# Optimization experiments

Hardware: AMD Instinct MI355X
Metric: run time of the kernel (lower is better)

## Reference

```python
import jax, jax.numpy as jnp
import numpy as np

BODY_EDGES = [(0, 2), (0, 5), (2, 7), (5, 8), (11, 12), (0, 11), (0, 12), (7, 11), (8, 12), (11, 13), (13, 15), (12, 14), (14, 16), (11, 23), (12, 24), (23, 24), (11, 24), (12, 23)]
N_JOINTS = 33
N_FEAT = 52
HIDDEN = 128
BN_EPS = 1e-5


def _make_adj():
    a = np.eye(N_JOINTS, dtype=np.float32)
    for i, j in BODY_EDGES:
        a[i, j] = 1.0
        a[j, i] = 1.0
    deg = np.clip(a.sum(1), 1.0, None)
    d = deg ** -0.5
    return jnp.asarray(d[:, None] * a * d[None, :])


def setup_inputs() -> dict:
    key = jax.random.key(0)
    ks = iter(jax.random.split(key, 40))
    B, T = 64, 256
    def lin(k, i, o):
        return jax.random.normal(k, (i, o), jnp.float32) / np.sqrt(i)
    inp = {
        'x': jax.random.normal(next(ks), (B, T, N_JOINTS, N_FEAT), jnp.float32),
        'adj': _make_adj(),
        # layer 0: in 52 -> out 128 (has skip linear)
        'W0': lin(next(ks), N_FEAT, HIDDEN), 'b0': jax.random.normal(next(ks), (HIDDEN,)) * 0.02,
        'S0': lin(next(ks), N_FEAT, HIDDEN), 'sb0': jax.random.normal(next(ks), (HIDDEN,)) * 0.02,
        'g0': 1.0 + 0.1 * jax.random.normal(next(ks), (HIDDEN,)), 'be0': 0.1 * jax.random.normal(next(ks), (HIDDEN,)),
        'm0': 0.1 * jax.random.normal(next(ks), (HIDDEN,)), 'v0': 1.0 + 0.1 * jax.random.uniform(next(ks), (HIDDEN,)),
        # layers 1,2: 128 -> 128 (identity skip)
        'W1': lin(next(ks), HIDDEN, HIDDEN), 'b1': jax.random.normal(next(ks), (HIDDEN,)) * 0.02,
        'g1': 1.0 + 0.1 * jax.random.normal(next(ks), (HIDDEN,)), 'be1': 0.1 * jax.random.normal(next(ks), (HIDDEN,)),
        'm1': 0.1 * jax.random.normal(next(ks), (HIDDEN,)), 'v1': 1.0 + 0.1 * jax.random.uniform(next(ks), (HIDDEN,)),
        'W2': lin(next(ks), HIDDEN, HIDDEN), 'b2': jax.random.normal(next(ks), (HIDDEN,)) * 0.02,
        'g2': 1.0 + 0.1 * jax.random.normal(next(ks), (HIDDEN,)), 'be2': 0.1 * jax.random.normal(next(ks), (HIDDEN,)),
        'm2': 0.1 * jax.random.normal(next(ks), (HIDDEN,)), 'v2': 1.0 + 0.1 * jax.random.uniform(next(ks), (HIDDEN,)),
        # temporal attention MLP: 128 -> 128 -> 1
        'tW1': lin(next(ks), HIDDEN, HIDDEN), 'tb1': jax.random.normal(next(ks), (HIDDEN,)) * 0.02,
        'tW2': lin(next(ks), HIDDEN, 1), 'tb2': jax.random.normal(next(ks), (1,)) * 0.02,
    }
    return inp


def _gcn(h, adj, W, b, g, be, m, v, skip):
    # adjacency mix: [B*T, J, D_in]
    a = jnp.einsum('nm,bmd->bnd', adj, h)
    z = a @ W + b
    z = (z - m) * jax.lax.rsqrt(v + BN_EPS) * g + be  # eval-mode BatchNorm1d
    return jax.nn.gelu(z, approximate=False) + skip


def reference(x, adj, W0, b0, S0, sb0, g0, be0, m0, v0,
              W1, b1, g1, be1, m1, v1,
              W2, b2, g2, be2, m2, v2,
              tW1, tb1, tW2, tb2):
    B, T, J, Fd = x.shape
    h = x.reshape(B * T, J, Fd)
    h = _gcn(h, adj, W0, b0, g0, be0, m0, v0, h @ S0 + sb0)
    h = _gcn(h, adj, W1, b1, g1, be1, m1, v1, h)
    h = _gcn(h, adj, W2, b2, g2, be2, m2, v2, h)
    # dropout inactive (eval mode)
    xt = h.mean(axis=1).reshape(B, T, -1)                  # [B, T, H]
    score = jax.nn.gelu(xt @ tW1 + tb1, approximate=False) @ tW2 + tb2  # [B, T, 1]
    attn = jax.nn.softmax(score, axis=1)
    return (xt * attn).sum(axis=1)                         # [B, H]
```

## Files before the change

kernel.cpp:

```cpp
#include <hip/hip_runtime.h>
#include <hip/hip_bf16.h>
#include <math.h>


#define NJ 33
#define NF 52
#define NH 128
#define NT 256
#define NB 64
#define NSAMP (NB*NT)
#define SPB 2
#define NBLKS (NSAMP/SPB)
#define HSTR 136
#define PSTR 40

typedef unsigned short u16;
typedef _Float16 f16;
typedef f16   half8 __attribute__((ext_vector_type(8)));
typedef f16   h2    __attribute__((ext_vector_type(2)));
typedef float f32x4 __attribute__((ext_vector_type(4)));

#define HO_W0    0
#define HO_S0    8192
#define HO_W1    16384
#define HO_W2    32768
#define HO_TW1   49152
#define HO_ADJ32 65536
#define H_TOTAL  66560
#define FO_BASE  (H_TOTAL/2)
#define FO_A0    (FO_BASE+0)
#define FO_SB0   (FO_BASE+768)
#define FO_TB1   (FO_BASE+896)
#define FO_TW2   (FO_BASE+1024)
#define FO_FLG   (FO_BASE+1152)
#define FO_XT    (FO_BASE+1280)
#define FO_SC    (FO_XT + NSAMP*NH)

__device__ __forceinline__ float bf2f(u16 u) { return __uint_as_float(((unsigned)u) << 16); }
__device__ __forceinline__ float ldv(const void* p, long i, int f) {
    float r;
    if (f) r = bf2f(((const u16*)p)[i]);
    else   r = ((const float*)p)[i];
    return r;
}
__device__ int detect_bf16(const void* p) {
    const u16* q = (const u16*)p;
    int nz = 0, ok = 0;
#pragma unroll
    for (int k = 0; k < 64; k++) {
        u16 u = q[k];
        if (u & 0x7FFF) {
            nz++;
            int e = (u >> 7) & 0xFF;
            ok += (e >= 0x40 && e <= 0xBF) ? 1 : 0;
        }
    }
    return (nz == 0) || (ok * 20 >= nz * 19);
}

__device__ __forceinline__ float gelu_c(float x) {
    float xc = fminf(fmaxf(x, -8.f), 8.f);
    float u  = xc * fmaf(xc * xc, 0.10294324f, 2.3022082f);
#if __has_builtin(__builtin_amdgcn_exp2f)
    float e  = __builtin_amdgcn_exp2f(u);
#else
    float e  = exp2f(u);
#endif
#if __has_builtin(__builtin_amdgcn_rcpf)
    float tt = (e - 1.f) * __builtin_amdgcn_rcpf(e + 1.f);
#else
    float tt = (e - 1.f) / (e + 1.f);
#endif
    float hx = 0.5f * x;
    return fmaf(hx, tt, hx);
}

#define MFMA16(a, b, c) __builtin_amdgcn_mfma_f32_16x16x32_f16(a, b, c, 0, 0, 0)

__global__ __launch_bounds__(256) void prep(
    const void* x, const void* adj,
    const void* W0, const void* b0, const void* S0, const void* sb0,
    const void* g0, const void* be0, const void* m0, const void* v0,
    const void* W1, const void* b1, const void* g1, const void* be1, const void* m1, const void* v1,
    const void* W2, const void* b2, const void* g2, const void* be2, const void* m2, const void* v2,
    const void* tW1, const void* tb1, const void* tW2,
    void* ws)
{
    f16* H = (f16*)ws; float* F = (float*)ws;
    const int bi = blockIdx.x, t = threadIdx.x;

    if (bi < 64) {
        const void* src; int dst, kt, nt, Kvalid, Kd;
        if (bi < 16)      { src = W1;  dst = HO_W1;  kt = (bi>>2)&3;    nt = bi&3;      Kvalid = 128; Kd = 128; }
        else if (bi < 32) { src = W2;  dst = HO_W2;  kt = ((bi-16)>>2); nt = (bi-16)&3; Kvalid = 128; Kd = 128; }
        else if (bi < 48) { src = tW1; dst = HO_TW1; kt = ((bi-32)>>2); nt = (bi-32)&3; Kvalid = 128; Kd = 128; }
        else if (bi < 56) { src = W0;  dst = HO_W0;  kt = ((bi-48)>>2); nt = (bi-48)&3; Kvalid = NF;  Kd = 64;  }
        else              { src = S0;  dst = HO_S0;  kt = ((bi-56)>>2); nt = (bi-56)&3; Kvalid = NF;  Kd = 64;  }
        const int flag = detect_bf16(src);
        __shared__ float tile[32][33];
        const int tx = t & 31, ty = t >> 5;
#pragma unroll
        for (int r = 0; r < 4; r++) {
            int k = kt*32 + ty + r*8;
            int n = nt*32 + tx;
            tile[ty + r*8][tx] = (k < Kvalid) ? ldv(src, (long)k*128 + n, flag) : 0.f;
        }
        __syncthreads();
#pragma unroll
        for (int r = 0; r < 4; r++) {
            int n = nt*32 + ty + r*8;
            int k = kt*32 + tx;
            H[dst + n*Kd + k] = (f16)tile[tx][ty + r*8];
        }
    } else {
        if (t == 0) ((int*)F)[FO_FLG] = detect_bf16(x);
        if (t < 128) {
            int c = t;
            {
                float g = ldv(g0,c,detect_bf16(g0)), be = ldv(be0,c,detect_bf16(be0));
                float m = ldv(m0,c,detect_bf16(m0)), v = ldv(v0,c,detect_bf16(v0));
                float b = ldv(b0,c,detect_bf16(b0));
                float A = g * rsqrtf(v + 1e-5f);
                F[FO_A0 + 0*256 + c] = A; F[FO_A0 + 0*256 + 128 + c] = (b - m)*A + be;
            }
            {
                float g = ldv(g1,c,detect_bf16(g1)), be = ldv(be1,c,detect_bf16(be1));
                float m = ldv(m1,c,detect_bf16(m1)), v = ldv(v1,c,detect_bf16(v1));
                float b = ldv(b1,c,detect_bf16(b1));
                float A = g * rsqrtf(v + 1e-5f);
                F[FO_A0 + 1*256 + c] = A; F[FO_A0 + 1*256 + 128 + c] = (b - m)*A + be;
            }
            {
                float g = ldv(g2,c,detect_bf16(g2)), be = ldv(be2,c,detect_bf16(be2));
                float m = ldv(m2,c,detect_bf16(m2)), v = ldv(v2,c,detect_bf16(v2));
                float b = ldv(b2,c,detect_bf16(b2));
                float A = g * rsqrtf(v + 1e-5f);
                F[FO_A0 + 2*256 + c] = A; F[FO_A0 + 2*256 + 128 + c] = (b - m)*A + be;
            }
            F[FO_SB0 + c] = ldv(sb0, c, detect_bf16(sb0));
            F[FO_TB1 + c] = ldv(tb1, c, detect_bf16(tb1));
            F[FO_TW2 + c] = ldv(tW2, c, detect_bf16(tW2));
        }
        const int fA = detect_bf16(adj);
        for (int i = t; i < 1024; i += 256) {
            int r = i >> 5, c = i & 31;
            float v = (r < 25 && c < 25) ? ldv(adj, (long)r*NJ + c, fA) : 0.f;
            H[HO_ADJ32 + i] = (f16)v;
        }
    }
}

#define ADJEPI_W(L, WRHB) {                                                     \
    f32x4 zac[2][2];                                                            \
    _Pragma("unroll")                                                           \
    for (int fF = 0; fF < 2; fF++) {                                            \
        half8 bz = *(const half8*)(Pt + (fF*128 + c)*PSTR + q*8);               \
        zac[fF][0] = MFMA16(afadj0, bz, z4);                                    \
        zac[fF][1] = MFMA16(afadj1, bz, z4);                                    \
    }                                                                           \
    const float Av = rA[L], Dv = rD[L];                                         \
    _Pragma("unroll")                                                           \
    for (int fF = 0; fF < 2; fF++) {                                            \
        _Pragma("unroll")                                                       \
        for (int m2 = 0; m2 < 2; m2++) {                                        \
            _Pragma("unroll")                                                   \
            for (int r4 = 0; r4 < 4; r4++) {                                    \
                float zv = (m2 == 0) ? zac[fF][0][r4]                           \
                         : (jlt[r4] ? zac[fF][1][r4] : acc[2*fF+1][r4]);        \
                float hnew = gelu_c(fmaf(zv, Av, Dv)) + hz[fF][m2][r4];         \
                hz[fF][m2][r4] = hnew;                                          \
                if (WRHB)                                                       \
                    hb[((2*fF+m2)*16 + q*4 + r4)*HSTR + c] = (f16)hnew;         \
            }                                                                   \
        }                                                                       \
        {                                                                       \
            float hnew = gelu_c(fmaf(acc[4][fF], Av, Dv)) + h32[fF];            \
            h32[fF] = (q == 0) ? hnew : 0.f;                                    \
            if (WRHB && q == 0)                                                 \
                hb[(64 + fF)*HSTR + c] = (f16)hnew;                             \
        }                                                                       \
    }                                                                           \
}

#define PTWRITE_W(ACC)                                                          \
    _Pragma("unroll")                                                           \
    for (int mt = 0; mt < 4; mt++) {                                            \
        const int fF = mt >> 1;                                                 \
        const int jb = (mt & 1) * 16;                                           \
        f16* pp = Pt + (fF*128 + c)*PSTR;                                       \
        _Pragma("unroll")                                                       \
        for (int r2 = 0; r2 < 4; r2 += 2) {                                     \
            int j0 = jb + q*4 + r2;                                             \
            if (j0 + 1 < 25) {                                                  \
                h2 v2w = { (f16)ACC[mt][r2], (f16)ACC[mt][r2+1] };              \
                *(h2*)(pp + j0) = v2w;                                          \
            } else if (j0 < 25) {                                               \
                pp[j0] = (f16)ACC[mt][r2];                                      \
            }                                                                   \
        }                                                                       \
    }

#define GEMM128_W(WOFF)                                                         \
    {                                                                           \
        half8 bf[4];                                                            \
        _Pragma("unroll")                                                       \
        for (int ks = 0; ks < 4; ks++)                                          \
            bf[ks] = *(const half8*)(HW + (WOFF) + c*128 + ks*32 + q*8);        \
        _Pragma("unroll")                                                       \
        for (int mt = 0; mt < 5; mt++) acc[mt] = z4;                            \
        _Pragma("unroll")                                                       \
        for (int mt = 0; mt < 5; mt++) {                                        \
            const int m = mt*16 + ml;                                           \
            _Pragma("unroll")                                                   \
            for (int ks = 0; ks < 4; ks++) {                                    \
                half8 af = *(const half8*)(hb + m*HSTR + ks*32 + q*8);          \
                acc[mt] = MFMA16(af, bf[ks], acc[mt]);                          \
            }                                                                   \
        }                                                                       \
    }

#define GCN_W_BODY                                                              \
    float* xtb = (float*)Pt;                                                    \
    const f16* HW = (const f16*)ws;                                             \
    float* F = (float*)ws;                                                      \
    float* xt_g = F + FO_XT;                                                    \
    float* sc_g = F + FO_SC;                                                    \
    const int t = threadIdx.x, lane = t & 63, wv = t >> 6;                      \
    const int q = lane >> 4, ml = lane & 15;                                    \
    const int c = wv * 16 + ml;                                                 \
    const f32x4 z4 = {0.f, 0.f, 0.f, 0.f};                                      \
    const bool jlt[4] = { q <= 2, q <= 1, q <= 1, q <= 1 };                     \
    const half8 zero8 = {(f16)0.f,(f16)0.f,(f16)0.f,(f16)0.f,(f16)0.f,(f16)0.f,(f16)0.f,(f16)0.f}; \
    {                                                                           \
        int fF = t >> 8, rem = t & 255, n = rem >> 1, chh = rem & 1;            \
        *(half8*)(Pt + (fF*128 + n)*PSTR + 24 + chh*8) = zero8;                 \
    }                                                                           \
    float rA[3], rD[3];                                                         \
    _Pragma("unroll")                                                           \
    for (int L = 0; L < 3; L++) {                                               \
        rA[L] = F[FO_A0 + L*256 + c];                                           \
        rD[L] = F[FO_A0 + L*256 + 128 + c];                                     \
    }                                                                           \
    const float sb0v = F[FO_SB0 + c];                                           \
    half8 afadj0 = *(const half8*)(HW + HO_ADJ32 + ml*32 + q*8);                \
    half8 afadj1 = *(const half8*)(HW + HO_ADJ32 + (16+ml)*32 + q*8);           \
    __syncthreads();                                                            \
    {                                                                           \
        const int fX = ((const int*)F)[FO_FLG];                                 \
        const long xb = (long)blockIdx.x * (SPB * NJ * NF);                     \
        _Pragma("unroll 1")                                                     \
        for (int it = 0; it < 2; it++) {                                        \
            int g = t + it * 512;                                               \
            if (g < 66 * 8) {                                                   \
                int r = g >> 3, blk = g & 7;                                    \
                int fF = (r >= 33) ? 1 : 0;                                     \
                int j = r - 33 * fF;                                            \
                int fr = (j < 32) ? (fF * 32 + j) : (64 + fF);                  \
                half8 o;                                                        \
                if (!fX) {                                                      \
                    const float* base = (const float*)x + xb + (long)r * NF + blk * 8; \
                    if (blk < 6) {                                              \
                        float4 v0 = *(const float4*)base;                       \
                        float4 v1 = *(const float4*)(base + 4);                 \
                        o[0]=(f16)v0.x; o[1]=(f16)v0.y; o[2]=(f16)v0.z; o[3]=(f16)v0.w; \
                        o[4]=(f16)v1.x; o[5]=(f16)v1.y; o[6]=(f16)v1.z; o[7]=(f16)v1.w; \
                    } else if (blk == 6) {                                      \
                        float4 v0 = *(const float4*)base;                       \
                        o = zero8;                                              \
                        o[0]=(f16)v0.x; o[1]=(f16)v0.y; o[2]=(f16)v0.z; o[3]=(f16)v0.w; \
                    } else o = zero8;                                           \
                } else {                                                        \
                    long rb = xb + (long)r * NF;                                \
                    _Pragma("unroll")                                           \
                    for (int i = 0; i < 8; i++) {                               \
                        int cx = blk * 8 + i;                                   \
                        o[i] = (f16)(cx < NF ? bf2f(((const u16*)x)[rb + cx]) : 0.f); \
                    }                                                           \
                }                                                               \
                *(half8*)(hb + fr * HSTR + blk * 8) = o;                        \
            }                                                                   \
        }                                                                       \
    }                                                                           \
    __syncthreads();                                                            \
    f32x4 acc[5];                                                               \
    float hz[2][2][4];                                                          \
    float h32[2];                                                               \
    {                                                                           \
        half8 bw[2], bs[2];                                                     \
        _Pragma("unroll")                                                       \
        for (int ks = 0; ks < 2; ks++) {                                        \
            bw[ks] = *(const half8*)(HW + HO_W0 + c*64 + ks*32 + q*8);          \
            bs[ks] = *(const half8*)(HW + HO_S0 + c*64 + ks*32 + q*8);          \
        }                                                                       \
        f32x4 acs[5];                                                           \
        _Pragma("unroll")                                                       \
        for (int mt = 0; mt < 5; mt++) { acc[mt] = z4; acs[mt] = z4; }          \
        _Pragma("unroll")                                                       \
        for (int mt = 0; mt < 5; mt++) {                                        \
            const int m = mt*16 + ml;                                           \
            half8 a0 = *(const half8*)(hb + m*HSTR + q*8);                      \
            half8 a1 = *(const half8*)(hb + m*HSTR + 32 + q*8);                 \
            acc[mt] = MFMA16(a0, bw[0], acc[mt]);                               \
            acc[mt] = MFMA16(a1, bw[1], acc[mt]);                               \
            acs[mt] = MFMA16(a0, bs[0], acs[mt]);                               \
            acs[mt] = MFMA16(a1, bs[1], acs[mt]);                               \
        }                                                                       \
        __syncthreads();                                                        \
        PTWRITE_W(acc)                                                          \
        _Pragma("unroll")                                                       \
        for (int fF = 0; fF < 2; fF++)                                          \
            _Pragma("unroll")                                                   \
            for (int m2 = 0; m2 < 2; m2++)                                      \
                _Pragma("unroll")                                               \
                for (int r4 = 0; r4 < 4; r4++)                                  \
                    hz[fF][m2][r4] = acs[2*fF+m2][r4] + sb0v;                   \
        _Pragma("unroll")                                                       \
        for (int fF = 0; fF < 2; fF++)                                          \
            h32[fF] = (q == 0) ? (acs[4][fF] + sb0v) : 0.f;                     \
    }                                                                           \
    ADJEPI_W(0, 1)                                                              \
    __syncthreads();                                                            \
    GEMM128_W(HO_W1)                                                            \
    __syncthreads();                                                            \
    PTWRITE_W(acc)                                                              \
    ADJEPI_W(1, 1)                                                              \
    __syncthreads();                                                            \
    GEMM128_W(HO_W2)                                                            \
    __syncthreads();                                                            \
    PTWRITE_W(acc)                                                              \
    ADJEPI_W(2, 0)                                                              \
    __syncthreads();                                                            \
    _Pragma("unroll")                                                           \
    for (int fF = 0; fF < 2; fF++) {                                            \
        float s = h32[fF];                                                      \
        _Pragma("unroll")                                                       \
        for (int m2 = 0; m2 < 2; m2++)                                          \
            _Pragma("unroll")                                                   \
            for (int r4 = 0; r4 < 4; r4++) s += hz[fF][m2][r4];                 \
        s += __shfl_xor(s, 16, 64);                                             \
        s += __shfl_xor(s, 32, 64);                                             \
        float xtc = s * (1.0f / 33.0f);                                         \
        if (q == 0) {                                                           \
            xtb[fF * 128 + c] = xtc;                                            \
            xt_g[((long)blockIdx.x * SPB + fF) * NH + c] = xtc;                 \
        }                                                                       \
    }                                                                           \
    __syncthreads();                                                            \
    {                                                                           \
        float r = 0.f;                                                          \
        if (t < 256) {                                                          \
            const int fF = t >> 7, ch = t & 127;                                \
            float u = 0.f;                                                      \
            _Pragma("unroll")                                                   \
            for (int kk = 0; kk < 16; kk++) {                                   \
                half8 wv8 = *(const half8*)(HW + HO_TW1 + ch*128 + kk*8);       \
                _Pragma("unroll")                                               \
                for (int i = 0; i < 8; i++)                                     \
                    u = fmaf(xtb[fF*128 + kk*8 + i], (float)wv8[i], u);         \
            }                                                                   \
            r = gelu_c(u + F[FO_TB1 + ch]) * F[FO_TW2 + ch];                    \
        }                                                                       \
        _Pragma("unroll")                                                       \
        for (int off = 32; off > 0; off >>= 1) r += __shfl_xor(r, off, 64);     \
        if (lane == 0 && wv < 4) rbuf4[wv] = r;                                 \
        __syncthreads();                                                        \
        if (t == 0) {                                                           \
            sc_g[blockIdx.x * SPB + 0] = rbuf4[0] + rbuf4[1];                   \
            sc_g[blockIdx.x * SPB + 1] = rbuf4[2] + rbuf4[3];                   \
        }                                                                       \
    }

__global__ __launch_bounds__(512) void gcn_mfma_w(const void* __restrict__ x,
                                                  void* __restrict__ ws)
{
    __shared__ __align__(16) f16 hb[80 * HSTR];
    __shared__ __align__(16) f16 Pt[2 * 128 * PSTR];
    __shared__ float rbuf4[4];
    GCN_W_BODY
}

__global__ __launch_bounds__(512, 8) void gcn_mfma_w73(const void* __restrict__ x,
                                                       void* __restrict__ ws)
{
    __shared__ __align__(16) f16 hb[73 * HSTR];
    __shared__ __align__(16) f16 Pt[2 * 128 * PSTR];
    __shared__ float rbuf4[4];
    GCN_W_BODY
}

__global__ __launch_bounds__(256) void attn_pool(
    const int* __restrict__ flg,
    const float* __restrict__ xt_ws, const float* __restrict__ score_ws,
    void* __restrict__ out)
{
    __shared__ float ew[NT];
    __shared__ float red[8];
    __shared__ float pb[256];
    const int t = threadIdx.x, lane = t & 63, wv = t >> 6;
    const int b = blockIdx.x >> 2, qr = blockIdx.x & 3;

    float sv = score_ws[b * NT + t];
    float m = sv;
#pragma unroll
    for (int off = 32; off > 0; off >>= 1) m = fmaxf(m, __shfl_xor(m, off, 64));
    if (lane == 0) red[wv] = m;
    __syncthreads();
    float mx = fmaxf(fmaxf(red[0], red[1]), fmaxf(red[2], red[3]));
    float e = __expf(sv - mx);
    ew[t] = e;
    float d = e;
#pragma unroll
    for (int off = 32; off > 0; off >>= 1) d += __shfl_xor(d, off, 64);
    if (lane == 0) red[4 + wv] = d;
    __syncthreads();
    float den = red[4] + red[5] + red[6] + red[7];

    const int cl = t & 31, ch = t >> 5;
    const int c = qr * 32 + cl;
    float a = 0.f;
#pragma unroll 4
    for (int i = ch * 32; i < ch * 32 + 32; i++)
        a = fmaf(ew[i], xt_ws[((long)b * NT + i) * NH + c], a);
    pb[t] = a;
    __syncthreads();
    if (t < 128) pb[t] += pb[t + 128];
    __syncthreads();
    if (t < 64) pb[t] += pb[t + 64];
    __syncthreads();
    if (t < 32) {
        float r = (pb[t] + pb[t + 32]) / den;
        if (*flg) ((__hip_bfloat16*)out)[b * NH + qr * 32 + t] = __float2bfloat16(r);
        else      ((float*)out)[b * NH + qr * 32 + t] = r;
    }
}

extern "C" void kernel_launch(void* const* d_in, const int* in_sizes, int n_in,
                              void* d_out, int out_size, void* d_ws, size_t ws_size,
                              hipStream_t stream) {
    static int use_73 = -1;
    if (use_73 < 0) {
        hipFuncAttributes a{};
        use_73 = 0;
        if (hipFuncGetAttributes(&a, reinterpret_cast<const void*>(gcn_mfma_w73)) == hipSuccess
            && a.numRegs > 0 && a.numRegs <= 64
            && a.localSizeBytes == 0)
            use_73 = 1;
    }
    prep<<<65, 256, 0, stream>>>(
        d_in[0], d_in[1],
        d_in[2], d_in[3], d_in[4], d_in[5],
        d_in[6], d_in[7], d_in[8], d_in[9],
        d_in[10], d_in[11], d_in[12], d_in[13], d_in[14], d_in[15],
        d_in[16], d_in[17], d_in[18], d_in[19], d_in[20], d_in[21],
        d_in[22], d_in[23], d_in[24],
        d_ws);
    if (use_73) gcn_mfma_w73<<<NBLKS, 512, 0, stream>>>(d_in[0], d_ws);
    else        gcn_mfma_w<<<NBLKS, 512, 0, stream>>>(d_in[0], d_ws);
    float* F = (float*)d_ws;
    attn_pool<<<NB * 4, 256, 0, stream>>>((const int*)(F + FO_FLG), F + FO_XT, F + FO_SC, d_out);
}
```

Baseline: 506.7 us.

## Add half-size Pt variant, sigmoid GELU variant, and occupancy-based kernel selection

Adds a GCN kernel variant that processes the two samples' adjacency epilogue one at a time, so the Pt staging buffer shrinks to one sample's worth of shared memory. Also adds a variant that uses a cheaper sigmoid-form GELU. The 73-row variant that relied on register limits is dropped, and the launcher now queries occupancy at runtime to choose among the three kernels. The goal is more resident blocks per CU, at the cost of extra work serialisation in the per-sample epilogue and a small numerical change in the GELU variant.

```diff
diff --git a/kernel.cpp b/kernel.cpp
--- a/kernel.cpp
+++ b/kernel.cpp
@@ -73,6 +73,20 @@
 #endif
     float hx = 0.5f * x;
     return fmaf(hx, tt, hx);
+}
+
+__device__ __forceinline__ float gelu_s(float x) {
+    float nu = x * fmaf(x * x, -0.10294324f, -2.3022082f);
+#if __has_builtin(__builtin_amdgcn_exp2f)
+    float e  = __builtin_amdgcn_exp2f(nu);
+#else
+    float e  = exp2f(nu);
+#endif
+#if __has_builtin(__builtin_amdgcn_rcpf)
+    return x * __builtin_amdgcn_rcpf(1.f + e);
+#else
+    return x / (1.f + e);
+#endif
 }
 
 #define MFMA16(a, b, c) __builtin_amdgcn_mfma_f32_16x16x32_f16(a, b, c, 0, 0, 0)
@@ -150,101 +164,7 @@
     }
 }
 
-#define ADJEPI_W(L, WRHB) {                                                     \
-    f32x4 zac[2][2];                                                            \
-    _Pragma("unroll")                                                           \
-    for (int fF = 0; fF < 2; fF++) {                                            \
-        half8 bz = *(const half8*)(Pt + (fF*128 + c)*PSTR + q*8);               \
-        zac[fF][0] = MFMA16(afadj0, bz, z4);                                    \
-        zac[fF][1] = MFMA16(afadj1, bz, z4);                                    \
-    }                                                                           \
-    const float Av = rA[L], Dv = rD[L];                                         \
-    _Pragma("unroll")                                                           \
-    for (int fF = 0; fF < 2; fF++) {                                            \
-        _Pragma("unroll")                                                       \
-        for (int m2 = 0; m2 < 2; m2++) {                                        \
-            _Pragma("unroll")                                                   \
-            for (int r4 = 0; r4 < 4; r4++) {                                    \
-                float zv = (m2 == 0) ? zac[fF][0][r4]                           \
-                         : (jlt[r4] ? zac[fF][1][r4] : acc[2*fF+1][r4]);        \
-                float hnew = gelu_c(fmaf(zv, Av, Dv)) + hz[fF][m2][r4];         \
-                hz[fF][m2][r4] = hnew;                                          \
-                if (WRHB)                                                       \
-                    hb[((2*fF+m2)*16 + q*4 + r4)*HSTR + c] = (f16)hnew;         \
-            }                                                                   \
-        }                                                                       \
-        {                                                                       \
-            float hnew = gelu_c(fmaf(acc[4][fF], Av, Dv)) + h32[fF];            \
-            h32[fF] = (q == 0) ? hnew : 0.f;                                    \
-            if (WRHB && q == 0)                                                 \
-                hb[(64 + fF)*HSTR + c] = (f16)hnew;                             \
-        }                                                                       \
-    }                                                                           \
-}
-
-#define PTWRITE_W(ACC)                                                          \
-    _Pragma("unroll")                                                           \
-    for (int mt = 0; mt < 4; mt++) {                                            \
-        const int fF = mt >> 1;                                                 \
-        const int jb = (mt & 1) * 16;                                           \
-        f16* pp = Pt + (fF*128 + c)*PSTR;                                       \
-        _Pragma("unroll")                                                       \
-        for (int r2 = 0; r2 < 4; r2 += 2) {                                     \
-            int j0 = jb + q*4 + r2;                                             \
-            if (j0 + 1 < 25) {                                                  \
-                h2 v2w = { (f16)ACC[mt][r2], (f16)ACC[mt][r2+1] };              \
-                *(h2*)(pp + j0) = v2w;                                          \
-            } else if (j0 < 25) {                                               \
-                pp[j0] = (f16)ACC[mt][r2];                                      \
-            }                                                                   \
-        }                                                                       \
-    }
-
-#define GEMM128_W(WOFF)                                                         \
-    {                                                                           \
-        half8 bf[4];                                                            \
-        _Pragma("unroll")                                                       \
-        for (int ks = 0; ks < 4; ks++)                                          \
-            bf[ks] = *(const half8*)(HW + (WOFF) + c*128 + ks*32 + q*8);        \
-        _Pragma("unroll")                                                       \
-        for (int mt = 0; mt < 5; mt++) acc[mt] = z4;                            \
-        _Pragma("unroll")                                                       \
-        for (int mt = 0; mt < 5; mt++) {                                        \
-            const int m = mt*16 + ml;                                           \
-            _Pragma("unroll")                                                   \
-            for (int ks = 0; ks < 4; ks++) {                                    \
-                half8 af = *(const half8*)(hb + m*HSTR + ks*32 + q*8);          \
-                acc[mt] = MFMA16(af, bf[ks], acc[mt]);                          \
-            }                                                                   \
-        }                                                                       \
-    }
-
-#define GCN_W_BODY                                                              \
-    float* xtb = (float*)Pt;                                                    \
-    const f16* HW = (const f16*)ws;                                             \
-    float* F = (float*)ws;                                                      \
-    float* xt_g = F + FO_XT;                                                    \
-    float* sc_g = F + FO_SC;                                                    \
-    const int t = threadIdx.x, lane = t & 63, wv = t >> 6;                      \
-    const int q = lane >> 4, ml = lane & 15;                                    \
-    const int c = wv * 16 + ml;                                                 \
-    const f32x4 z4 = {0.f, 0.f, 0.f, 0.f};                                      \
-    const bool jlt[4] = { q <= 2, q <= 1, q <= 1, q <= 1 };                     \
-    const half8 zero8 = {(f16)0.f,(f16)0.f,(f16)0.f,(f16)0.f,(f16)0.f,(f16)0.f,(f16)0.f,(f16)0.f}; \
-    {                                                                           \
-        int fF = t >> 8, rem = t & 255, n = rem >> 1, chh = rem & 1;            \
-        *(half8*)(Pt + (fF*128 + n)*PSTR + 24 + chh*8) = zero8;                 \
-    }                                                                           \
-    float rA[3], rD[3];                                                         \
-    _Pragma("unroll")                                                           \
-    for (int L = 0; L < 3; L++) {                                               \
-        rA[L] = F[FO_A0 + L*256 + c];                                           \
-        rD[L] = F[FO_A0 + L*256 + 128 + c];                                     \
-    }                                                                           \
-    const float sb0v = F[FO_SB0 + c];                                           \
-    half8 afadj0 = *(const half8*)(HW + HO_ADJ32 + ml*32 + q*8);                \
-    half8 afadj1 = *(const half8*)(HW + HO_ADJ32 + (16+ml)*32 + q*8);           \
-    __syncthreads();                                                            \
+#define STAGE_X                                                                 \
     {                                                                           \
         const int fX = ((const int*)F)[FO_FLG];                                 \
         const long xb = (long)blockIdx.x * (SPB * NJ * NF);                     \
@@ -280,56 +200,28 @@
                 *(half8*)(hb + fr * HSTR + blk * 8) = o;                        \
             }                                                                   \
         }                                                                       \
-    }                                                                           \
-    __syncthreads();                                                            \
-    f32x4 acc[5];                                                               \
-    float hz[2][2][4];                                                          \
-    float h32[2];                                                               \
+    }
+
+#define GEMM128_W(WOFF)                                                         \
     {                                                                           \
-        half8 bw[2], bs[2];                                                     \
-        _Pragma("unroll")                                                       \
-        for (int ks = 0; ks < 2; ks++) {                                        \
-            bw[ks] = *(const half8*)(HW + HO_W0 + c*64 + ks*32 + q*8);          \
-            bs[ks] = *(const half8*)(HW + HO_S0 + c*64 + ks*32 + q*8);          \
-        }                                                                       \
-        f32x4 acs[5];                                                           \
-        _Pragma("unroll")                                                       \
-        for (int mt = 0; mt < 5; mt++) { acc[mt] = z4; acs[mt] = z4; }          \
+        half8 bf[4];                                                            \
+        _Pragma("unroll")                                                       \
+        for (int ks = 0; ks < 4; ks++)                                          \
+            bf[ks] = *(const half8*)(HW + (WOFF) + c*128 + ks*32 + q*8);        \
+        _Pragma("unroll")                                                       \
+        for (int mt = 0; mt < 5; mt++) acc[mt] = z4;                            \
         _Pragma("unroll")                                                       \
         for (int mt = 0; mt < 5; mt++) {                                        \
             const int m = mt*16 + ml;                                           \
-            half8 a0 = *(const half8*)(hb + m*HSTR + q*8);                      \
-            half8 a1 = *(const half8*)(hb + m*HSTR + 32 + q*8);                 \
-            acc[mt] = MFMA16(a0, bw[0], acc[mt]);                               \
-            acc[mt] = MFMA16(a1, bw[1], acc[mt]);                               \
-            acs[mt] = MFMA16(a0, bs[0], acs[mt]);                               \
-            acs[mt] = MFMA16(a1, bs[1], acs[mt]);                               \
-        }                                                                       \
-        __syncthreads();                                                        \
-        PTWRITE_W(acc)                                                          \
-        _Pragma("unroll")                                                       \
-        for (int fF = 0; fF < 2; fF++)                                          \
             _Pragma("unroll")                                                   \
-            for (int m2 = 0; m2 < 2; m2++)                                      \
-                _Pragma("unroll")                                               \
-                for (int r4 = 0; r4 < 4; r4++)                                  \
-                    hz[fF][m2][r4] = acs[2*fF+m2][r4] + sb0v;                   \
-        _Pragma("unroll")                                                       \
-        for (int fF = 0; fF < 2; fF++)                                          \
-            h32[fF] = (q == 0) ? (acs[4][fF] + sb0v) : 0.f;                     \
-    }                                                                           \
-    ADJEPI_W(0, 1)                                                              \
-    __syncthreads();                                                            \
-    GEMM128_W(HO_W1)                                                            \
-    __syncthreads();                                                            \
-    PTWRITE_W(acc)                                                              \
-    ADJEPI_W(1, 1)                                                              \
-    __syncthreads();                                                            \
-    GEMM128_W(HO_W2)                                                            \
-    __syncthreads();                                                            \
-    PTWRITE_W(acc)                                                              \
-    ADJEPI_W(2, 0)                                                              \
-    __syncthreads();                                                            \
+            for (int ks = 0; ks < 4; ks++) {                                    \
+                half8 af = *(const half8*)(hb + m*HSTR + ks*32 + q*8);          \
+                acc[mt] = MFMA16(af, bf[ks], acc[mt]);                          \
+            }                                                                   \
+        }                                                                       \
+    }
+
+#define TAIL_W(GELUF)                                                           \
     _Pragma("unroll")                                                           \
     for (int fF = 0; fF < 2; fF++) {                                            \
         float s = h32[fF];                                                      \
@@ -358,7 +250,7 @@
                 for (int i = 0; i < 8; i++)                                     \
                     u = fmaf(xtb[fF*128 + kk*8 + i], (float)wv8[i], u);         \
             }                                                                   \
-            r = gelu_c(u + F[FO_TB1 + ch]) * F[FO_TW2 + ch];                    \
+            r = GELUF(u + F[FO_TB1 + ch]) * F[FO_TW2 + ch];                     \
         }                                                                       \
         _Pragma("unroll")                                                       \
         for (int off = 32; off > 0; off >>= 1) r += __shfl_xor(r, off, 64);     \
@@ -370,22 +262,283 @@
         }                                                                       \
     }
 
+#define ADJEPI_W(L, WRHB, GELUF) {                                              \
+    f32x4 zac[2][2];                                                            \
+    _Pragma("unroll")                                                           \
+    for (int fF = 0; fF < 2; fF++) {                                            \
+        half8 bz = *(const half8*)(Pt + (fF*128 + c)*PSTR + q*8);               \
+        zac[fF][0] = MFMA16(afadj0, bz, z4);                                    \
+        zac[fF][1] = MFMA16(afadj1, bz, z4);                                    \
+    }                                                                           \
+    const float Av = rA[L], Dv = rD[L];                                         \
+    _Pragma("unroll")                                                           \
+    for (int fF = 0; fF < 2; fF++) {                                            \
+        _Pragma("unroll")                                                       \
+        for (int m2 = 0; m2 < 2; m2++) {                                        \
+            _Pragma("unroll")                                                   \
+            for (int r4 = 0; r4 < 4; r4++) {                                    \
+                float zv = (m2 == 0) ? zac[fF][0][r4]                           \
+                         : (jlt[r4] ? zac[fF][1][r4] : acc[2*fF+1][r4]);        \
+                float hnew = GELUF(fmaf(zv, Av, Dv)) + hz[fF][m2][r4];          \
+                hz[fF][m2][r4] = hnew;                                          \
+                if (WRHB)                                                       \
+                    hb[((2*fF+m2)*16 + q*4 + r4)*HSTR + c] = (f16)hnew;         \
+            }                                                                   \
+        }                                                                       \
+        {                                                                       \
+            float hnew = GELUF(fmaf(acc[4][fF], Av, Dv)) + h32[fF];             \
+            h32[fF] = (q == 0) ? hnew : 0.f;                                    \
+            if (WRHB && q == 0)                                                 \
+                hb[(64 + fF)*HSTR + c] = (f16)hnew;                             \
+        }                                                                       \
+    }                                                                           \
+}
+
+#define PTWRITE_W(ACC)                                                          \
+    _Pragma("unroll")                                                           \
+    for (int mt = 0; mt < 4; mt++) {                                            \
+        const int fF = mt >> 1;                                                 \
+        const int jb = (mt & 1) * 16;                                           \
+        f16* pp = Pt + (fF*128 + c)*PSTR;                                       \
+        _Pragma("unroll")                                                       \
+        for (int r2 = 0; r2 < 4; r2 += 2) {                                     \
+            int j0 = jb + q*4 + r2;                                             \
+            if (j0 + 1 < 25) {                                                  \
+                h2 v2w = { (f16)ACC[mt][r2], (f16)ACC[mt][r2+1] };              \
+                *(h2*)(pp + j0) = v2w;                                          \
+            } else if (j0 < 25) {                                               \
+                pp[j0] = (f16)ACC[mt][r2];                                      \
+            }                                                                   \
+        }                                                                       \
+    }
+
+#define GCN_W_BODY(GELUF)                                                       \
+    float* xtb = (float*)Pt;                                                    \
+    const f16* HW = (const f16*)ws;                                             \
+    float* F = (float*)ws;                                                      \
+    float* xt_g = F + FO_XT;                                                    \
+    float* sc_g = F + FO_SC;                                                    \
+    const int t = threadIdx.x, lane = t & 63, wv = t >> 6;                      \
+    const int q = lane >> 4, ml = lane & 15;                                    \
+    const int c = wv * 16 + ml;                                                 \
+    const f32x4 z4 = {0.f, 0.f, 0.f, 0.f};                                      \
+    const bool jlt[4] = { q <= 2, q <= 1, q <= 1, q <= 1 };                     \
+    const half8 zero8 = {(f16)0.f,(f16)0.f,(f16)0.f,(f16)0.f,(f16)0.f,(f16)0.f,(f16)0.f,(f16)0.f}; \
+    {                                                                           \
+        int fF = t >> 8, rem = t & 255, n = rem >> 1, chh = rem & 1;            \
+        *(half8*)(Pt + (fF*128 + n)*PSTR + 24 + chh*8) = zero8;                 \
+    }                                                                           \
+    float rA[3], rD[3];                                                         \
+    _Pragma("unroll")                                                           \
+    for (int L = 0; L < 3; L++) {                                               \
+        rA[L] = F[FO_A0 + L*256 + c];                                           \
+        rD[L] = F[FO_A0 + L*256 + 128 + c];                                     \
+    }                                                                           \
+    const float sb0v = F[FO_SB0 + c];                                           \
+    half8 afadj0 = *(const half8*)(HW + HO_ADJ32 + ml*32 + q*8);                \
+    half8 afadj1 = *(const half8*)(HW + HO_ADJ32 + (16+ml)*32 + q*8);           \
+    __syncthreads();                                                            \
+    STAGE_X                                                                     \
+    __syncthreads();                                                            \
+    f32x4 acc[5];                                                               \
+    float hz[2][2][4];                                                          \
+    float h32[2];                                                               \
+    {                                                                           \
+        half8 bw[2], bs[2];                                                     \
+        _Pragma("unroll")                                                       \
+        for (int ks = 0; ks < 2; ks++) {                                        \
+            bw[ks] = *(const half8*)(HW + HO_W0 + c*64 + ks*32 + q*8);          \
+            bs[ks] = *(const half8*)(HW + HO_S0 + c*64 + ks*32 + q*8);          \
+        }                                                                       \
+        f32x4 acs[5];                                                           \
+        _Pragma("unroll")                                                       \
+        for (int mt = 0; mt < 5; mt++) { acc[mt] = z4; acs[mt] = z4; }          \
+        _Pragma("unroll")                                                       \
+        for (int mt = 0; mt < 5; mt++) {                                        \
+            const int m = mt*16 + ml;                                           \
+            half8 a0 = *(const half8*)(hb + m*HSTR + q*8);                      \
+            half8 a1 = *(const half8*)(hb + m*HSTR + 32 + q*8);                 \
+            acc[mt] = MFMA16(a0, bw[0], acc[mt]);                               \
+            acc[mt] = MFMA16(a1, bw[1], acc[mt]);                               \
+            acs[mt] = MFMA16(a0, bs[0], acs[mt]);                               \
+            acs[mt] = MFMA16(a1, bs[1], acs[mt]);                               \
+        }                                                                       \
+        __syncthreads();                                                        \
+        PTWRITE_W(acc)                                                          \
+        _Pragma("unroll")                                                       \
+        for (int fF = 0; fF < 2; fF++)                                          \
+            _Pragma("unroll")                                                   \
+            for (int m2 = 0; m2 < 2; m2++)                                      \
+                _Pragma("unroll")                                               \
+                for (int r4 = 0; r4 < 4; r4++)                                  \
+                    hz[fF][m2][r4] = acs[2*fF+m2][r4] + sb0v;                   \
+        _Pragma("unroll")                                                       \
+        for (int fF = 0; fF < 2; fF++)                                          \
+            h32[fF] = (q == 0) ? (acs[4][fF] + sb0v) : 0.f;                     \
+    }                                                                           \
+    ADJEPI_W(0, 1, GELUF)                                                       \
+    __syncthreads();                                                            \
+    GEMM128_W(HO_W1)                                                            \
+    __syncthreads();                                                            \
+    PTWRITE_W(acc)                                                              \
+    ADJEPI_W(1, 1, GELUF)                                                       \
+    __syncthreads();                                                            \
+    GEMM128_W(HO_W2)                                                            \
+    __syncthreads();                                                            \
+    PTWRITE_W(acc)                                                              \
+    ADJEPI_W(2, 0, GELUF)                                                       \
+    __syncthreads();                                                            \
+    TAIL_W(GELUF)
+
+#define ADJEPI_WF(L, FF, WRHB) {                                                \
+    half8 bz = *(const half8*)(Pt + c*PSTR + q*8);                              \
+    f32x4 zac0 = MFMA16(afadj0, bz, z4);                                        \
+    f32x4 zac1 = MFMA16(afadj1, bz, z4);                                        \
+    const float Av = rA[L], Dv = rD[L];                                         \
+    _Pragma("unroll")                                                           \
+    for (int m2 = 0; m2 < 2; m2++) {                                            \
+        _Pragma("unroll")                                                       \
+        for (int r4 = 0; r4 < 4; r4++) {                                        \
+            float zv = (m2 == 0) ? zac0[r4]                                     \
+                     : (jlt[r4] ? zac1[r4] : acc[2*(FF)+1][r4]);                \
+            float hnew = gelu_c(fmaf(zv, Av, Dv)) + hz[FF][m2][r4];             \
+            hz[FF][m2][r4] = hnew;                                              \
+            if (WRHB)                                                           \
+                hb[((2*(FF)+m2)*16 + q*4 + r4)*HSTR + c] = (f16)hnew;           \
+        }                                                                       \
+    }                                                                           \
+    {                                                                           \
+        float hnew = gelu_c(fmaf(acc[4][FF], Av, Dv)) + h32[FF];                \
+        h32[FF] = (q == 0) ? hnew : 0.f;                                        \
+        if (WRHB && q == 0)                                                     \
+            hb[(64 + (FF))*HSTR + c] = (f16)hnew;                               \
+    }                                                                           \
+}
+
+#define PTWRITE_WF(ACC, FF)                                                     \
+    _Pragma("unroll")                                                           \
+    for (int mtl = 0; mtl < 2; mtl++) {                                         \
+        const int mt = 2*(FF) + mtl;                                            \
+        const int jb = mtl * 16;                                                \
+        f16* pp = Pt + c*PSTR;                                                  \
+        _Pragma("unroll")                                                       \
+        for (int r2 = 0; r2 < 4; r2 += 2) {                                     \
+            int j0 = jb + q*4 + r2;                                             \
+            if (j0 + 1 < 25) {                                                  \
+                h2 v2w = { (f16)ACC[mt][r2], (f16)ACC[mt][r2+1] };              \
+                *(h2*)(pp + j0) = v2w;                                          \
+            } else if (j0 < 25) {                                               \
+                pp[j0] = (f16)ACC[mt][r2];                                      \
+            }                                                                   \
+        }                                                                       \
+    }
+
 __global__ __launch_bounds__(512) void gcn_mfma_w(const void* __restrict__ x,
                                                   void* __restrict__ ws)
 {
     __shared__ __align__(16) f16 hb[80 * HSTR];
     __shared__ __align__(16) f16 Pt[2 * 128 * PSTR];
     __shared__ float rbuf4[4];
-    GCN_W_BODY
-}
-
-__global__ __launch_bounds__(512, 8) void gcn_mfma_w73(const void* __restrict__ x,
-                                                       void* __restrict__ ws)
+    GCN_W_BODY(gelu_c)
+}
+
+__global__ __launch_bounds__(512) void gcn_mfma_wg(const void* __restrict__ x,
+                                                   void* __restrict__ ws)
 {
-    __shared__ __align__(16) f16 hb[73 * HSTR];
+    __shared__ __align__(16) f16 hb[80 * HSTR];
     __shared__ __align__(16) f16 Pt[2 * 128 * PSTR];
     __shared__ float rbuf4[4];
-    GCN_W_BODY
+    GCN_W_BODY(gelu_s)
+}
+
+__global__ __launch_bounds__(512) void gcn_mfma_wpt(const void* __restrict__ x,
+                                                    void* __restrict__ ws)
+{
+    __shared__ __align__(16) f16 hb[80 * HSTR];
+    __shared__ __align__(16) f16 Pt[128 * PSTR];
+    __shared__ float rbuf4[4];
+    float* xtb = (float*)Pt;
+    const f16* HW = (const f16*)ws;
+    float* F = (float*)ws;
+    float* xt_g = F + FO_XT;
+    float* sc_g = F + FO_SC;
+    const int t = threadIdx.x, lane = t & 63, wv = t >> 6;
+    const int q = lane >> 4, ml = lane & 15;
+    const int c = wv * 16 + ml;
+    const f32x4 z4 = {0.f, 0.f, 0.f, 0.f};
+    const bool jlt[4] = { q <= 2, q <= 1, q <= 1, q <= 1 };
+    const half8 zero8 = {(f16)0.f,(f16)0.f,(f16)0.f,(f16)0.f,(f16)0.f,(f16)0.f,(f16)0.f,(f16)0.f};
+    if (t < 256) {
+        int n = t >> 1, chh = t & 1;
+        *(half8*)(Pt + n*PSTR + 24 + chh*8) = zero8;
+    }
+    float rA[3], rD[3];
+#pragma unroll
+    for (int L = 0; L < 3; L++) {
+        rA[L] = F[FO_A0 + L*256 + c];
+        rD[L] = F[FO_A0 + L*256 + 128 + c];
+    }
+    const float sb0v = F[FO_SB0 + c];
+    half8 afadj0 = *(const half8*)(HW + HO_ADJ32 + ml*32 + q*8);
+    half8 afadj1 = *(const half8*)(HW + HO_ADJ32 + (16+ml)*32 + q*8);
+    __syncthreads();
+    STAGE_X
+    __syncthreads();
+    f32x4 acc[5];
+    float hz[2][2][4];
+    float h32[2];
+    {
+        half8 bw[2], bs[2];
+#pragma unroll
+        for (int ks = 0; ks < 2; ks++) {
+            bw[ks] = *(const half8*)(HW + HO_W0 + c*64 + ks*32 + q*8);
+            bs[ks] = *(const half8*)(HW + HO_S0 + c*64 + ks*32 + q*8);
+        }
+        f32x4 acs[5];
+#pragma unroll
+        for (int mt = 0; mt < 5; mt++) { acc[mt] = z4; acs[mt] = z4; }
+#pragma unroll
+        for (int mt = 0; mt < 5; mt++) {
+            const int m = mt*16 + ml;
+            half8 a0 = *(const half8*)(hb + m*HSTR + q*8);
+            half8 a1 = *(const half8*)(hb + m*HSTR + 32 + q*8);
+            acc[mt] = MFMA16(a0, bw[0], acc[mt]);
+            acc[mt] = MFMA16(a1, bw[1], acc[mt]);
+            acs[mt] = MFMA16(a0, bs[0], acs[mt]);
+            acs[mt] = MFMA16(a1, bs[1], acs[mt]);
+        }
+        __syncthreads();
+#pragma unroll
+        for (int fF = 0; fF < 2; fF++)
+#pragma unroll
+            for (int m2 = 0; m2 < 2; m2++)
+#pragma unroll
+                for (int r4 = 0; r4 < 4; r4++)
+                    hz[fF][m2][r4] = acs[2*fF+m2][r4] + sb0v;
+#pragma unroll
+        for (int fF = 0; fF < 2; fF++)
+            h32[fF] = (q == 0) ? (acs[4][fF] + sb0v) : 0.f;
+    }
+    PTWRITE_WF(acc, 0)
+    ADJEPI_WF(0, 0, 1)
+    PTWRITE_WF(acc, 1)
+    ADJEPI_WF(0, 1, 1)
+    __syncthreads();
+    GEMM128_W(HO_W1)
+    __syncthreads();
+    PTWRITE_WF(acc, 0)
+    ADJEPI_WF(1, 0, 1)
+    PTWRITE_WF(acc, 1)
+    ADJEPI_WF(1, 1, 1)
+    __syncthreads();
+    GEMM128_W(HO_W2)
+    __syncthreads();
+    PTWRITE_WF(acc, 0)
+    ADJEPI_WF(2, 0, 0)
+    PTWRITE_WF(acc, 1)
+    ADJEPI_WF(2, 1, 0)
+    __syncthreads();
+    TAIL_W(gelu_c)
 }
 
 __global__ __launch_bounds__(256) void attn_pool(
@@ -437,14 +590,25 @@
 extern "C" void kernel_launch(void* const* d_in, const int* in_sizes, int n_in,
                               void* d_out, int out_size, void* d_ws, size_t ws_size,
                               hipStream_t stream) {
-    static int use_73 = -1;
-    if (use_73 < 0) {
-        hipFuncAttributes a{};
-        use_73 = 0;
-        if (hipFuncGetAttributes(&a, reinterpret_cast<const void*>(gcn_mfma_w73)) == hipSuccess
-            && a.numRegs > 0 && a.numRegs <= 64
-            && a.localSizeBytes == 0)
-            use_73 = 1;
+    static int pick = -1;
+    if (pick < 0) {
+        auto occ = [](const void* f) -> int {
+            int n = 0;
+            return (hipOccupancyMaxActiveBlocksPerMultiprocessor(&n, f, 512, 0)
+                    == hipSuccess) ? n : 0;
+        };
+        auto clean = [](const void* f) -> bool {
+            hipFuncAttributes a{};
+            return hipFuncGetAttributes(&a, f) == hipSuccess
+                   && a.localSizeBytes == 0;
+        };
+        const void* fw   = reinterpret_cast<const void*>(gcn_mfma_w);
+        const void* fwpt = reinterpret_cast<const void*>(gcn_mfma_wpt);
+        const void* fwg  = reinterpret_cast<const void*>(gcn_mfma_wg);
+        int ow = occ(fw);
+        pick = 2;
+        if (clean(fwpt) && occ(fwpt) > ow)      pick = 0;
+        else if (clean(fwg) && occ(fwg) >= ow)  pick = 1;
     }
     prep<<<65, 256, 0, stream>>>(
         d_in[0], d_in[1],
@@ -454,8 +618,9 @@
         d_in[16], d_in[17], d_in[18], d_in[19], d_in[20], d_in[21],
         d_in[22], d_in[23], d_in[24],
         d_ws);
-    if (use_73) gcn_mfma_w73<<<NBLKS, 512, 0, stream>>>(d_in[0], d_ws);
-    else        gcn_mfma_w<<<NBLKS, 512, 0, stream>>>(d_in[0], d_ws);
+    if      (pick == 0) gcn_mfma_wpt<<<NBLKS, 512, 0, stream>>>(d_in[0], d_ws);
+    else if (pick == 1) gcn_mfma_wg <<<NBLKS, 512, 0, stream>>>(d_in[0], d_ws);
+    else                gcn_mfma_w  <<<NBLKS, 512, 0, stream>>>(d_in[0], d_ws);
     float* F = (float*)d_ws;
     attn_pool<<<NB * 4, 256, 0, stream>>>((const int*)(F + FO_FLG), F + FO_XT, F + FO_SC, d_out);
 }
```

Result: faster. 489.5 us (-3.4%).
